# Kernel tuning notes

Hardware: AMD Instinct MI355X
Metric: run time of the kernel (lower is better)

Reference implementation:

```python
import jax, jax.numpy as jnp
import numpy as np

S = 7; B = 2; C = 20; N = 8; BS = 16384
LAMBDA_COORD = 5.0; LAMBDA_NOOBJ = 0.5
EPS = 1e-6


def setup_inputs() -> dict:
    key = jax.random.key(0)
    k1, k2, k3 = jax.random.split(key, 3)
    outputs = jax.random.uniform(k1, (BS, S, S, B * 5 + C), dtype=jnp.float32)
    gt_boxes = jax.random.uniform(k2, (BS, N, 4), dtype=jnp.float32)
    gt_labels = jax.random.randint(k3, (BS, N), 0, C)
    return {"outputs": outputs, "gt_boxes": gt_boxes, "gt_labels": gt_labels}


def _pairwise_iou(pred_xywh, gt_boxes):
    # pred_xywh: [bs,S,S,B,4] (center x,y,w,h); gt_boxes: [bs,N,4] -> iou [bs,S,S,B,N]
    p = pred_xywh[..., None, :]                       # [bs,S,S,B,1,4]
    g = gt_boxes[:, None, None, None, :, :]           # [bs,1,1,1,N,4]
    px1, py1 = p[..., 0] - p[..., 2] / 2, p[..., 1] - p[..., 3] / 2
    px2, py2 = p[..., 0] + p[..., 2] / 2, p[..., 1] + p[..., 3] / 2
    gx1, gy1 = g[..., 0] - g[..., 2] / 2, g[..., 1] - g[..., 3] / 2
    gx2, gy2 = g[..., 0] + g[..., 2] / 2, g[..., 1] + g[..., 3] / 2
    iw = jnp.clip(jnp.minimum(px2, gx2) - jnp.maximum(px1, gx1), 0.0)
    ih = jnp.clip(jnp.minimum(py2, gy2) - jnp.maximum(py1, gy1), 0.0)
    inter = iw * ih
    union = p[..., 2] * p[..., 3] + g[..., 2] * g[..., 3] - inter
    return inter / (union + EPS)


def reference(outputs, gt_boxes, gt_labels):
    bs = outputs.shape[0]
    pred = outputs[..., : B * 5].reshape(bs, S, S, B, 5)   # [bs,S,S,B,5]
    pred_xywh, pred_conf = pred[..., :4], pred[..., 4]
    pred_cls = outputs[..., B * 5:]                        # [bs,S,S,C]

    iou = _pairwise_iou(pred_xywh, gt_boxes)               # [bs,S,S,B,N]

    # Original loop: for each gt j, if iou(:,j).max() > best -> best_iou, best_box_idx = argmax over B.
    iou_max_over_b = jnp.max(iou, axis=3)                  # [bs,S,S,N]
    j_star = jnp.argmax(iou_max_over_b, axis=-1)
    best_iou = jnp.max(iou_max_over_b, axis=-1)            # [bs,S,S]
    iou_at_j = jnp.take_along_axis(iou, j_star[..., None, None], axis=4)[..., 0]  # [bs,S,S,B]
    best_b = jnp.argmax(iou_at_j, axis=-1)                 # [bs,S,S] in [0,B)

    # Faithful to source: gt_boxes indexed by best_box_idx (the pred-box index), requires N >= B.
    gt_sel = jnp.take_along_axis(
        jnp.broadcast_to(gt_boxes[:, None, None], (bs, S, S, N, 4)),
        best_b[..., None, None], axis=3)[..., 0, :]        # [bs,S,S,4]
    pred_sel = jnp.take_along_axis(pred, best_b[..., None, None], axis=3)[..., 0, :]  # [bs,S,S,5]

    loc = ((pred_sel[..., 0] - gt_sel[..., 0]) ** 2
           + (pred_sel[..., 1] - gt_sel[..., 1]) ** 2
           + (jnp.sqrt(pred_sel[..., 2]) - jnp.sqrt(gt_sel[..., 2])) ** 2
           + (jnp.sqrt(pred_sel[..., 3]) - jnp.sqrt(gt_sel[..., 3])) ** 2)
    loc = LAMBDA_COORD * loc                               # [bs,S,S]

    conf_obj = (pred_sel[..., 4] - best_iou) ** 2          # [bs,S,S]

    # Classification: mean cross-entropy of the cell's class logits vs all gt labels
    logp = jax.nn.log_softmax(pred_cls, axis=-1)           # [bs,S,S,C]
    lab = jnp.broadcast_to(gt_labels[:, None, None, :], (bs, S, S, N))
    ce = -jnp.mean(jnp.take_along_axis(logp, lab, axis=3), axis=-1)  # [bs,S,S]

    noobj = LAMBDA_NOOBJ * jnp.sum(pred_conf ** 2, axis=-1)  # [bs,S,S]

    has_obj = best_iou > 0.0
    per_cell = jnp.where(has_obj, loc + conf_obj + ce, noobj)
    return jnp.sum(per_cell) / bs
```

## Files before the change

### kernel.cpp

```cpp
#include <hip/hip_runtime.h>

namespace {

constexpr int kS = 7;
constexpr int kC = 20;
constexpr int kN = 8;
constexpr int kBS = 16384;
constexpr int kCells = kBS * kS * kS;
constexpr int kWT = 64;
constexpr int kNT = kCells / kWT;
constexpr int kGrid = 2560;
constexpr int kF = 30;
constexpr float kLambdaCoord = 5.0f;
constexpr float kLambdaNoobj = 0.5f;
constexpr float kEps = 1e-6f;

typedef const __attribute__((address_space(1))) unsigned int gu32;
typedef __attribute__((address_space(3))) unsigned int lu32;

__device__ __forceinline__ void stage(const float* __restrict__ outputs,
                                      int t, float* dst, int lane) {
  const char* srcb =
      reinterpret_cast<const char*>(outputs) + (size_t)t * kWT * 120;
  char* dstb = reinterpret_cast<char*>(dst);
#pragma unroll
  for (int k = 0; k < 7; ++k) {
    __builtin_amdgcn_global_load_lds((gu32*)(srcb + k * 1024 + lane * 16),
                                     (lu32*)(dstb + k * 1024 + lane * 16),
                                     16, 0, 0);
  }
  if (lane < 32) {
    __builtin_amdgcn_global_load_lds((gu32*)(srcb + 7168 + lane * 16),
                                     (lu32*)(dstb + 7168 + lane * 16),
                                     16, 0, 0);
  }
}

__global__ __launch_bounds__(64) void yolo_loss_kernel(
    const float* __restrict__ outputs,
    const float* __restrict__ gt_boxes,
    const int* __restrict__ gt_labels,
    float* __restrict__ partials) {
  __shared__ float lds[2][kWT * kF];

  const int lane = threadIdx.x;
  float val = 0.0f;

  int t = blockIdx.x;
  int cur = 0;
  stage(outputs, t, lds[0], lane);

  while (t < kNT) {
    const int nxt = t + kGrid;

    const int c = t * kWT + lane;
    const int bs = c / (kS * kS);
    float g[kN][4];
    const float4* gb4 =
        reinterpret_cast<const float4*>(gt_boxes + (size_t)bs * kN * 4);
#pragma unroll
    for (int n = 0; n < kN; ++n) {
      float4 v = gb4[n];
      g[n][0] = v.x; g[n][1] = v.y; g[n][2] = v.z; g[n][3] = v.w;
    }
    const int4* lb4 = reinterpret_cast<const int4*>(gt_labels + (size_t)bs * kN);
    const int4 lab0 = lb4[0];
    const int4 lab1 = lb4[1];

    if (nxt < kNT) {
      asm volatile("s_waitcnt lgkmcnt(0)" ::: "memory");
      stage(outputs, nxt, lds[cur ^ 1], lane);
    }

    float gx1[kN], gx2[kN], gy1[kN], gy2[kN], ga[kN];
#pragma unroll
    for (int n = 0; n < kN; ++n) {
      gx1[n] = g[n][0] - g[n][2] * 0.5f;
      gx2[n] = g[n][0] + g[n][2] * 0.5f;
      gy1[n] = g[n][1] - g[n][3] * 0.5f;
      gy2[n] = g[n][1] + g[n][3] * 0.5f;
      ga[n]  = g[n][2] * g[n][3];
    }

    if (nxt < kNT) {
      asm volatile("s_waitcnt vmcnt(8)" ::: "memory");
    } else {
      asm volatile("s_waitcnt vmcnt(0)" ::: "memory");
    }

    const float* x = &lds[cur][lane * kF];

    float iou[2][kN];
#pragma unroll
    for (int b = 0; b < 2; ++b) {
      const float px = x[b * 5 + 0], py = x[b * 5 + 1];
      const float pw = x[b * 5 + 2], ph = x[b * 5 + 3];
      const float px1 = px - pw * 0.5f, px2 = px + pw * 0.5f;
      const float py1 = py - ph * 0.5f, py2 = py + ph * 0.5f;
      const float parea = pw * ph;
#pragma unroll
      for (int n = 0; n < kN; ++n) {
        const float iw = fmaxf(fminf(px2, gx2[n]) - fmaxf(px1, gx1[n]), 0.0f);
        const float ih = fmaxf(fminf(py2, gy2[n]) - fmaxf(py1, gy1[n]), 0.0f);
        const float inter = iw * ih;
        const float uni = parea + ga[n] - inter;
        iou[b][n] = inter * __builtin_amdgcn_rcpf(uni + kEps);
      }
    }

    float best_iou = -1.0f;
    float i0j = 0.0f, i1j = 0.0f;
#pragma unroll
    for (int n = 0; n < kN; ++n) {
      const float m = fmaxf(iou[0][n], iou[1][n]);
      if (m > best_iou) { best_iou = m; i0j = iou[0][n]; i1j = iou[1][n]; }
    }
    const int bb = (i1j > i0j) ? 1 : 0;

    const float gsx = bb ? g[1][0] : g[0][0];
    const float gsy = bb ? g[1][1] : g[0][1];
    const float gsw = bb ? g[1][2] : g[0][2];
    const float gsh = bb ? g[1][3] : g[0][3];
    const float psx = bb ? x[5] : x[0];
    const float psy = bb ? x[6] : x[1];
    const float psw = bb ? x[7] : x[2];
    const float psh = bb ? x[8] : x[3];
    const float psc = bb ? x[9] : x[4];

    const float dx = psx - gsx;
    const float dy = psy - gsy;
    const float dw = __builtin_amdgcn_sqrtf(psw) - __builtin_amdgcn_sqrtf(gsw);
    const float dh = __builtin_amdgcn_sqrtf(psh) - __builtin_amdgcn_sqrtf(gsh);
    const float loc = kLambdaCoord * (dx * dx + dy * dy + dw * dw + dh * dh);
    const float conf_obj = (psc - best_iou) * (psc - best_iou);

    float se0 = 0.0f, se1 = 0.0f, se2 = 0.0f, se3 = 0.0f;
#pragma unroll
    for (int k = 0; k < kC; k += 4) {
      se0 += __expf(x[10 + k + 0]);
      se1 += __expf(x[10 + k + 1]);
      se2 += __expf(x[10 + k + 2]);
      se3 += __expf(x[10 + k + 3]);
    }
    const float lse = __logf((se0 + se1) + (se2 + se3));

    float s8 = 0.0f;
    s8 += x[10 + lab0.x] + x[10 + lab0.y] + x[10 + lab0.z] + x[10 + lab0.w];
    s8 += x[10 + lab1.x] + x[10 + lab1.y] + x[10 + lab1.z] + x[10 + lab1.w];
    const float ce = lse - 0.125f * s8;

    const float noobj = kLambdaNoobj * (x[4] * x[4] + x[9] * x[9]);

    val += (best_iou > 0.0f) ? (loc + conf_obj + ce) : noobj;

    t = nxt;
    cur ^= 1;
  }

#pragma unroll
  for (int off = 32; off > 0; off >>= 1) val += __shfl_down(val, off, 64);
  if (lane == 0) partials[blockIdx.x] = val;
}

__global__ __launch_bounds__(256) void reduce_kernel(
    const float* __restrict__ partials, float* __restrict__ out) {
  const float4* p4 = reinterpret_cast<const float4*>(partials);
  float s = 0.0f;
  for (int i = threadIdx.x; i < kGrid / 4; i += 256) {
    const float4 v = p4[i];
    s += (v.x + v.y) + (v.z + v.w);
  }
#pragma unroll
  for (int off = 32; off > 0; off >>= 1) s += __shfl_down(s, off, 64);
  __shared__ float ws[4];
  const int lane = threadIdx.x & 63;
  const int wid = threadIdx.x >> 6;
  if (lane == 0) ws[wid] = s;
  __syncthreads();
  if (threadIdx.x == 0) {
    out[0] = (ws[0] + ws[1] + ws[2] + ws[3]) * (1.0f / kBS);
  }
}

}

extern "C" void kernel_launch(void* const* d_in, const int* in_sizes, int n_in,
                              void* d_out, int out_size, void* d_ws, size_t ws_size,
                              hipStream_t stream) {
  const float* outputs = (const float*)d_in[0];
  const float* gt_boxes = (const float*)d_in[1];
  const int* gt_labels = (const int*)d_in[2];
  float* out = (float*)d_out;
  float* partials = (float*)d_ws;

  yolo_loss_kernel<<<kGrid, kWT, 0, stream>>>(outputs, gt_boxes, gt_labels, partials);
  reduce_kernel<<<1, 256, 0, stream>>>(partials, out);
}
```

Before: 28.05 us.

## Split each cell across two lanes, one per predicted box, with shuffle exchange

```diff
diff --git a/kernel.cpp b/kernel.cpp
--- a/kernel.cpp
+++ b/kernel.cpp
@@ -2,17 +2,16 @@
 
 namespace {
 
-constexpr int kS = 7;
 constexpr int kC = 20;
 constexpr int kN = 8;
 constexpr int kBS = 16384;
-constexpr int kCells = kBS * kS * kS;
-constexpr int kWT = 64;
-constexpr int kNT = kCells / kWT;
-constexpr int kGrid = 2560;
-constexpr int kF = 30;
-constexpr float kLambdaCoord = 5.0f;
-constexpr float kLambdaNoobj = 0.5f;
+constexpr int kCells = kBS * 49;
+constexpr int kCT = 32;
+constexpr int kNT = kCells / kCT;
+constexpr int kWaves = 5120;
+constexpr int kGrid = kWaves / 2;
+constexpr float kLC = 5.0f;
+constexpr float kLN = 0.5f;
 constexpr float kEps = 1e-6f;
 
 typedef const __attribute__((address_space(1))) unsigned int gu32;
@@ -21,40 +20,46 @@
 __device__ __forceinline__ void stage(const float* __restrict__ outputs,
                                       int t, float* dst, int lane) {
   const char* srcb =
-      reinterpret_cast<const char*>(outputs) + (size_t)t * kWT * 120;
+      reinterpret_cast<const char*>(outputs) + (size_t)t * (kCT * 120);
   char* dstb = reinterpret_cast<char*>(dst);
 #pragma unroll
-  for (int k = 0; k < 7; ++k) {
+  for (int k = 0; k < 3; ++k) {
     __builtin_amdgcn_global_load_lds((gu32*)(srcb + k * 1024 + lane * 16),
                                      (lu32*)(dstb + k * 1024 + lane * 16),
                                      16, 0, 0);
   }
-  if (lane < 32) {
-    __builtin_amdgcn_global_load_lds((gu32*)(srcb + 7168 + lane * 16),
-                                     (lu32*)(dstb + 7168 + lane * 16),
+  if (lane < 48) {
+    __builtin_amdgcn_global_load_lds((gu32*)(srcb + 3072 + lane * 16),
+                                     (lu32*)(dstb + 3072 + lane * 16),
                                      16, 0, 0);
   }
 }
 
-__global__ __launch_bounds__(64) void yolo_loss_kernel(
+__global__ __launch_bounds__(128) void yolo_loss_kernel(
     const float* __restrict__ outputs,
     const float* __restrict__ gt_boxes,
     const int* __restrict__ gt_labels,
     float* __restrict__ partials) {
-  __shared__ float lds[2][kWT * kF];
-
-  const int lane = threadIdx.x;
-  float val = 0.0f;
-
-  int t = blockIdx.x;
+  __shared__ float lds[2][2][kCT * 30];
+
+  const int tid = threadIdx.x;
+  const int lane = tid & 63;
+  const int wv = tid >> 6;
+  const int gw = blockIdx.x * 2 + wv;
+  const int ci = lane >> 1;
+  const int b = lane & 1;
+
+  float acc = 0.0f;
+  int t = gw;
   int cur = 0;
-  stage(outputs, t, lds[0], lane);
-
-  while (t < kNT) {
-    const int nxt = t + kGrid;
-
-    const int c = t * kWT + lane;
-    const int bs = c / (kS * kS);
+  stage(outputs, t, lds[wv][0], lane);
+
+  while (true) {
+    const int nxt = t + kWaves;
+    const bool more = nxt < kNT;
+
+    const int c = t * kCT + ci;
+    const int bs = c / 49;
     float g[kN][4];
     const float4* gb4 =
         reinterpret_cast<const float4*>(gt_boxes + (size_t)bs * kN * 4);
@@ -63,13 +68,12 @@
       float4 v = gb4[n];
       g[n][0] = v.x; g[n][1] = v.y; g[n][2] = v.z; g[n][3] = v.w;
     }
-    const int4* lb4 = reinterpret_cast<const int4*>(gt_labels + (size_t)bs * kN);
-    const int4 lab0 = lb4[0];
-    const int4 lab1 = lb4[1];
-
-    if (nxt < kNT) {
+    const int4 labA =
+        reinterpret_cast<const int4*>(gt_labels + (size_t)bs * kN)[b];
+
+    if (more) {
       asm volatile("s_waitcnt lgkmcnt(0)" ::: "memory");
-      stage(outputs, nxt, lds[cur ^ 1], lane);
+      stage(outputs, nxt, lds[wv][cur ^ 1], lane);
     }
 
     float gx1[kN], gx2[kN], gy1[kN], gy2[kN], ga[kN];
@@ -82,91 +86,97 @@
       ga[n]  = g[n][2] * g[n][3];
     }
 
-    if (nxt < kNT) {
-      asm volatile("s_waitcnt vmcnt(8)" ::: "memory");
+    if (more) {
+      asm volatile("s_waitcnt vmcnt(4)" ::: "memory");
     } else {
       asm volatile("s_waitcnt vmcnt(0)" ::: "memory");
     }
 
-    const float* x = &lds[cur][lane * kF];
-
-    float iou[2][kN];
-#pragma unroll
-    for (int b = 0; b < 2; ++b) {
-      const float px = x[b * 5 + 0], py = x[b * 5 + 1];
-      const float pw = x[b * 5 + 2], ph = x[b * 5 + 3];
-      const float px1 = px - pw * 0.5f, px2 = px + pw * 0.5f;
-      const float py1 = py - ph * 0.5f, py2 = py + ph * 0.5f;
-      const float parea = pw * ph;
-#pragma unroll
-      for (int n = 0; n < kN; ++n) {
-        const float iw = fmaxf(fminf(px2, gx2[n]) - fmaxf(px1, gx1[n]), 0.0f);
-        const float ih = fmaxf(fminf(py2, gy2[n]) - fmaxf(py1, gy1[n]), 0.0f);
-        const float inter = iw * ih;
-        const float uni = parea + ga[n] - inter;
-        iou[b][n] = inter * __builtin_amdgcn_rcpf(uni + kEps);
-      }
-    }
-
-    float best_iou = -1.0f;
-    float i0j = 0.0f, i1j = 0.0f;
-#pragma unroll
-    for (int n = 0; n < kN; ++n) {
-      const float m = fmaxf(iou[0][n], iou[1][n]);
-      if (m > best_iou) { best_iou = m; i0j = iou[0][n]; i1j = iou[1][n]; }
+    const float* x = &lds[wv][cur][ci * 30];
+
+    const float* wb = x + b * 5;
+    const float o0 = wb[0], o1 = wb[1], o2 = wb[2], o3 = wb[3], o4 = wb[4];
+    const float px1 = o0 - o2 * 0.5f, px2 = o0 + o2 * 0.5f;
+    const float py1 = o1 - o3 * 0.5f, py2 = o1 + o3 * 0.5f;
+    const float pa = o2 * o3;
+
+    float iouv[kN];
+#pragma unroll
+    for (int n = 0; n < kN; ++n) {
+      const float iw = fmaxf(fminf(px2, gx2[n]) - fmaxf(px1, gx1[n]), 0.0f);
+      const float ih = fmaxf(fminf(py2, gy2[n]) - fmaxf(py1, gy1[n]), 0.0f);
+      const float inter = iw * ih;
+      iouv[n] = inter * __builtin_amdgcn_rcpf(pa + ga[n] - inter + kEps);
+    }
+
+    float best = -1.0f, i0j = 0.0f, i1j = 0.0f;
+#pragma unroll
+    for (int n = 0; n < kN; ++n) {
+      const float other = __shfl_xor(iouv[n], 1, 64);
+      const float i0 = b ? other : iouv[n];
+      const float i1 = b ? iouv[n] : other;
+      const float m = fmaxf(i0, i1);
+      if (m > best) { best = m; i0j = i0; i1j = i1; }
     }
     const int bb = (i1j > i0j) ? 1 : 0;
+
+    const float q0 = __shfl_xor(o0, 1, 64), q1 = __shfl_xor(o1, 1, 64),
+                q2 = __shfl_xor(o2, 1, 64), q3 = __shfl_xor(o3, 1, 64),
+                q4 = __shfl_xor(o4, 1, 64);
+    const bool own_chosen = (bb == b);
+    const float psx = own_chosen ? o0 : q0;
+    const float psy = own_chosen ? o1 : q1;
+    const float psw = own_chosen ? o2 : q2;
+    const float psh = own_chosen ? o3 : q3;
+    const float psc = own_chosen ? o4 : q4;
 
     const float gsx = bb ? g[1][0] : g[0][0];
     const float gsy = bb ? g[1][1] : g[0][1];
-    const float gsw = bb ? g[1][2] : g[0][2];
-    const float gsh = bb ? g[1][3] : g[0][3];
-    const float psx = bb ? x[5] : x[0];
-    const float psy = bb ? x[6] : x[1];
-    const float psw = bb ? x[7] : x[2];
-    const float psh = bb ? x[8] : x[3];
-    const float psc = bb ? x[9] : x[4];
-
+    const float sgw = __builtin_amdgcn_sqrtf(bb ? g[1][2] : g[0][2]);
+    const float sgh = __builtin_amdgcn_sqrtf(bb ? g[1][3] : g[0][3]);
     const float dx = psx - gsx;
     const float dy = psy - gsy;
-    const float dw = __builtin_amdgcn_sqrtf(psw) - __builtin_amdgcn_sqrtf(gsw);
-    const float dh = __builtin_amdgcn_sqrtf(psh) - __builtin_amdgcn_sqrtf(gsh);
-    const float loc = kLambdaCoord * (dx * dx + dy * dy + dw * dw + dh * dh);
-    const float conf_obj = (psc - best_iou) * (psc - best_iou);
-
-    float se0 = 0.0f, se1 = 0.0f, se2 = 0.0f, se3 = 0.0f;
-#pragma unroll
-    for (int k = 0; k < kC; k += 4) {
-      se0 += __expf(x[10 + k + 0]);
-      se1 += __expf(x[10 + k + 1]);
-      se2 += __expf(x[10 + k + 2]);
-      se3 += __expf(x[10 + k + 3]);
-    }
-    const float lse = __logf((se0 + se1) + (se2 + se3));
-
-    float s8 = 0.0f;
-    s8 += x[10 + lab0.x] + x[10 + lab0.y] + x[10 + lab0.z] + x[10 + lab0.w];
-    s8 += x[10 + lab1.x] + x[10 + lab1.y] + x[10 + lab1.z] + x[10 + lab1.w];
+    const float dw = __builtin_amdgcn_sqrtf(psw) - sgw;
+    const float dh = __builtin_amdgcn_sqrtf(psh) - sgh;
+    const float loc = kLC * (dx * dx + dy * dy + dw * dw + dh * dh);
+    const float conf_obj = (psc - best) * (psc - best);
+
+    const float2* cp = reinterpret_cast<const float2*>(x + 10 + b * 10);
+    float s0 = 0.0f, s1 = 0.0f;
+#pragma unroll
+    for (int j = 0; j < 5; ++j) {
+      const float2 v = cp[j];
+      s0 += __expf(v.x);
+      s1 += __expf(v.y);
+    }
+    const float seh = s0 + s1;
+    const float lse = __logf(seh + __shfl_xor(seh, 1, 64));
+
+    const float s4 =
+        x[10 + labA.x] + x[10 + labA.y] + x[10 + labA.z] + x[10 + labA.w];
+    const float s8 = s4 + __shfl_xor(s4, 1, 64);
     const float ce = lse - 0.125f * s8;
 
-    const float noobj = kLambdaNoobj * (x[4] * x[4] + x[9] * x[9]);
-
-    val += (best_iou > 0.0f) ? (loc + conf_obj + ce) : noobj;
-
+    const float noobj = kLN * (o4 * o4 + q4 * q4);
+
+    const float val = (best > 0.0f) ? (loc + conf_obj + ce) : noobj;
+    if (b == 0) acc += val;
+
+    if (!more) break;
     t = nxt;
     cur ^= 1;
   }
 
 #pragma unroll
-  for (int off = 32; off > 0; off >>= 1) val += __shfl_down(val, off, 64);
-  if (lane == 0) partials[blockIdx.x] = val;
+  for (int off = 32; off > 0; off >>= 1) acc += __shfl_down(acc, off, 64);
+  if (lane == 0) partials[gw] = acc;
 }
 
 __global__ __launch_bounds__(256) void reduce_kernel(
     const float* __restrict__ partials, float* __restrict__ out) {
   const float4* p4 = reinterpret_cast<const float4*>(partials);
   float s = 0.0f;
-  for (int i = threadIdx.x; i < kGrid / 4; i += 256) {
+  for (int i = threadIdx.x; i < kWaves / 4; i += 256) {
     const float4 v = p4[i];
     s += (v.x + v.y) + (v.z + v.w);
   }
@@ -193,6 +203,6 @@
   float* out = (float*)d_out;
   float* partials = (float*)d_ws;
 
-  yolo_loss_kernel<<<kGrid, kWT, 0, stream>>>(outputs, gt_boxes, gt_labels, partials);
+  yolo_loss_kernel<<<kGrid, 128, 0, stream>>>(outputs, gt_boxes, gt_labels, partials);
   reduce_kernel<<<1, 256, 0, stream>>>(partials, out);
 }
```

Result: slower. 28.74 us (+2.5%).
